# Performance work log

Hardware: AMD Instinct MI355X
Metric: run time of the kernel (lower is better)

## Reference

```python
import jax, jax.numpy as jnp
import numpy as np

B, E, D = 4096, 64, 1024

def setup_inputs() -> dict:
    key = jax.random.key(0)
    k1, k2 = jax.random.split(key)
    z = jax.random.normal(k1, (B, D), dtype=jnp.float32)
    expert_keys = jax.random.normal(k2, (E, D), dtype=jnp.float32)
    log_sigma = jnp.zeros((D,), dtype=jnp.float32)
    return {"z": z, "expert_keys": expert_keys, "log_sigma": log_sigma}

def reference(z, expert_keys, log_sigma):
    # diag(sigma_inv) @ diff followed by (. * diff).sum(-1) is exactly an
    # elementwise-scaled squared distance: sum_d exp(-log_sigma_d) * diff_d^2
    sigma_inv = jnp.exp(-log_sigma)                              # [D]
    diff = z[:, None, :] - expert_keys[None, :, :]               # [B, E, D]
    mahalanobis_dist = jnp.einsum('bed,d,bed->be', diff, sigma_inv, diff)  # [B, E]
    similarity = 1.0 / (1.0 + mahalanobis_dist)                  # [B, E]
    weights = jax.nn.softmax(similarity, axis=-1)                # [B, E]
    weighted_expert = weights @ expert_keys                      # [B, D]
    return (similarity, weighted_expert)
```

## Files before the change

### kernel.cpp

```cpp
#include <hip/hip_runtime.h>
#include <hip/hip_bf16.h>

#define B_N 4096
#define E_N 64
#define D_N 1024
#define ROWS 16

typedef __bf16 bf16x8 __attribute__((ext_vector_type(8)));
typedef __bf16 bf16x4 __attribute__((ext_vector_type(4)));
typedef float f32x4 __attribute__((ext_vector_type(4)));


__global__ __launch_bounds__(256) void prep_kernel(
    const float* __restrict__ keys, const float* __restrict__ lsig,
    float* __restrict__ sinv, float* __restrict__ ak,
    __bf16* __restrict__ sk, __bf16* __restrict__ kT)
{
  __shared__ float red[4];
  __shared__ __bf16 tl[64][72];
  const int bid = blockIdx.x;
  const int t = threadIdx.x;

  if (bid < 64) {
    const int e = bid;
    const float4 k4 = *(const float4*)(keys + e * D_N + 4 * t);
    const float4 l4 = *(const float4*)(lsig + 4 * t);
    float4 s4;
    s4.x = expf(-l4.x); s4.y = expf(-l4.y); s4.z = expf(-l4.z); s4.w = expf(-l4.w);
    if (e == 0) *(float4*)(sinv + 4 * t) = s4;
    const float4 sk4 = make_float4(s4.x * k4.x, s4.y * k4.y, s4.z * k4.z, s4.w * k4.w);
    bf16x4 skb;
    skb[0] = (__bf16)sk4.x; skb[1] = (__bf16)sk4.y; skb[2] = (__bf16)sk4.z; skb[3] = (__bf16)sk4.w;
    *(bf16x4*)(sk + e * D_N + 4 * t) = skb;
    float p = sk4.x * k4.x + sk4.y * k4.y + sk4.z * k4.z + sk4.w * k4.w;
    #pragma unroll
    for (int off = 32; off > 0; off >>= 1) p += __shfl_down(p, off);
    if ((t & 63) == 0) red[t >> 6] = p;
    __syncthreads();
    if (t == 0) ak[e] = red[0] + red[1] + red[2] + red[3];
  } else {
    const int d0 = (bid - 64) * 64;
    #pragma unroll
    for (int p = 0; p < 4; ++p) {
      const int e  = p * 16 + (t >> 4);
      const int dd = (t & 15) * 4;
      const float4 k4 = *(const float4*)(keys + (size_t)e * D_N + d0 + dd);
      tl[dd + 0][e] = (__bf16)k4.x; tl[dd + 1][e] = (__bf16)k4.y;
      tl[dd + 2][e] = (__bf16)k4.z; tl[dd + 3][e] = (__bf16)k4.w;
    }
    __syncthreads();
    #pragma unroll
    for (int p = 0; p < 2; ++p) {
      const int dd = p * 32 + (t >> 3);
      const int l8 = t & 7;
      const bf16x8 v = *(const bf16x8*)&tl[dd][l8 * 8];
      *(bf16x8*)(kT + (size_t)(d0 + dd) * E_N + l8 * 8) = v;
    }
  }
}

__global__ __launch_bounds__(256) void main_kernel(
    const float* __restrict__ z, const float* __restrict__ sinv,
    const float* __restrict__ ak, const __bf16* __restrict__ sk,
    const __bf16* __restrict__ kT,
    float* __restrict__ out_sim, float* __restrict__ out_we)
{
  constexpr int ZS = D_N + 8;
  __shared__ __bf16 zlds[ROWS * ZS];
  __shared__ float azs[ROWS];
  __shared__ float simb[ROWS][68];
  __shared__ __bf16 wlds[ROWS][72];

  const int t  = threadIdx.x;
  const int b0 = blockIdx.x * ROWS;
  const int wave = t >> 6;
  const int lane = t & 63;
  const int ln = lane & 15;
  const int q  = lane >> 4;

  const int sr = t >> 4;
  const int sc = t & 15;
  const float* zrow = z + (size_t)(b0 + sr) * D_N;
  float az = 0.f;
  #pragma unroll
  for (int l = 0; l < 8; ++l) {
    const int c = sc * 4 + l * 64;
    const float4 z4 = *(const float4*)(zrow + c);
    const float4 s4 = *(const float4*)(sinv + c);
    az += s4.x * z4.x * z4.x + s4.y * z4.y * z4.y + s4.z * z4.z * z4.z + s4.w * z4.w * z4.w;
    bf16x4 zb;
    zb[0] = (__bf16)z4.x; zb[1] = (__bf16)z4.y; zb[2] = (__bf16)z4.z; zb[3] = (__bf16)z4.w;
    *(bf16x4*)(&zlds[sr * ZS + c]) = zb;
  }
  const float akv = ak[wave * 16 + ln];
  __syncthreads();

  f32x4 acc = {0.f, 0.f, 0.f, 0.f};
  const __bf16* bp = sk + (size_t)(wave * 16 + ln) * D_N + q * 8;
  const __bf16* ap = &zlds[ln * ZS + q * 8];
  {
    float4 z4b[4], s4b[4];
    #pragma unroll
    for (int l = 0; l < 4; ++l) {
      const int c = 512 + sc * 4 + l * 64;
      z4b[l] = *(const float4*)(zrow + c);
      s4b[l] = *(const float4*)(sinv + c);
    }
    #pragma unroll
    for (int ks = 0; ks < 16; ++ks) {
      const bf16x8 bfr = *(const bf16x8*)(bp + ks * 32);
      const bf16x8 afr = *(const bf16x8*)(ap + ks * 32);
      acc = __builtin_amdgcn_mfma_f32_16x16x32_bf16(afr, bfr, acc, 0, 0, 0);
    }
    #pragma unroll
    for (int l = 0; l < 4; ++l) {
      const int c = 512 + sc * 4 + l * 64;
      const float4 z4 = z4b[l], s4 = s4b[l];
      az += s4.x * z4.x * z4.x + s4.y * z4.y * z4.y + s4.z * z4.z * z4.z + s4.w * z4.w * z4.w;
      bf16x4 zb;
      zb[0] = (__bf16)z4.x; zb[1] = (__bf16)z4.y; zb[2] = (__bf16)z4.z; zb[3] = (__bf16)z4.w;
      *(bf16x4*)(&zlds[sr * ZS + c]) = zb;
    }
    #pragma unroll
    for (int l = 0; l < 4; ++l) {
      const int c = 768 + sc * 4 + l * 64;
      const float4 z4 = *(const float4*)(zrow + c);
      const float4 s4 = *(const float4*)(sinv + c);
      az += s4.x * z4.x * z4.x + s4.y * z4.y * z4.y + s4.z * z4.z * z4.z + s4.w * z4.w * z4.w;
      bf16x4 zb;
      zb[0] = (__bf16)z4.x; zb[1] = (__bf16)z4.y; zb[2] = (__bf16)z4.z; zb[3] = (__bf16)z4.w;
      *(bf16x4*)(&zlds[sr * ZS + c]) = zb;
    }
  }
  az += __shfl_xor(az, 1); az += __shfl_xor(az, 2);
  az += __shfl_xor(az, 4); az += __shfl_xor(az, 8);
  if (sc == 0) azs[sr] = az;
  __syncthreads();

  #pragma unroll
  for (int ks = 16; ks < 32; ++ks) {
    const bf16x8 bfr = *(const bf16x8*)(bp + ks * 32);
    const bf16x8 afr = *(const bf16x8*)(ap + ks * 32);
    acc = __builtin_amdgcn_mfma_f32_16x16x32_bf16(afr, bfr, acc, 0, 0, 0);
  }
  #pragma unroll
  for (int i = 0; i < 4; ++i) {
    const int row = q * 4 + i;
    const float dist = azs[row] + akv - 2.0f * acc[i];
    simb[row][wave * 16 + ln] = 1.0f / (1.0f + dist);
  }
  const __bf16* kp0 = kT + (size_t)(wave * 256 + ln) * E_N + q * 8;
  const bf16x8 pa0 = *(const bf16x8*)(kp0);
  const bf16x8 pa1 = *(const bf16x8*)(kp0 + 32);
  __syncthreads();

  {
    const int row = wave * 4 + q;
    const f32x4 v4 = *(const f32x4*)&simb[row][ln * 4];
    float mx = fmaxf(fmaxf(v4[0], v4[1]), fmaxf(v4[2], v4[3]));
    mx = fmaxf(mx, __shfl_xor(mx, 1)); mx = fmaxf(mx, __shfl_xor(mx, 2));
    mx = fmaxf(mx, __shfl_xor(mx, 4)); mx = fmaxf(mx, __shfl_xor(mx, 8));
    float e0 = __expf(v4[0] - mx), e1 = __expf(v4[1] - mx);
    float e2 = __expf(v4[2] - mx), e3 = __expf(v4[3] - mx);
    float sum = e0 + e1 + e2 + e3;
    sum += __shfl_xor(sum, 1); sum += __shfl_xor(sum, 2);
    sum += __shfl_xor(sum, 4); sum += __shfl_xor(sum, 8);
    const float inv = 1.0f / sum;
    bf16x4 wv;
    wv[0] = (__bf16)(e0 * inv); wv[1] = (__bf16)(e1 * inv);
    wv[2] = (__bf16)(e2 * inv); wv[3] = (__bf16)(e3 * inv);
    *(bf16x4*)&wlds[row][ln * 4] = wv;
  }
  __syncthreads();

  {
    const float4 sv = *(const float4*)&simb[t >> 4][(t & 15) * 4];
    *(float4*)(out_sim + (size_t)(b0 + (t >> 4)) * E_N + (t & 15) * 4) = sv;
  }

  const bf16x8 wb0 = *(const bf16x8*)&wlds[ln][q * 8];
  const bf16x8 wb1 = *(const bf16x8*)&wlds[ln][32 + q * 8];
  float* orow = out_we + (size_t)(b0 + ln) * D_N + wave * 256 + q * 4;
  #pragma unroll
  for (int i = 0; i < 16; ++i) {
    const int d0 = wave * 256 + i * 16;
    bf16x8 a0f, a1f;
    if (i == 0) { a0f = pa0; a1f = pa1; }
    else {
      const __bf16* kp = kT + (size_t)(d0 + ln) * E_N + q * 8;
      a0f = *(const bf16x8*)(kp);
      a1f = *(const bf16x8*)(kp + 32);
    }
    f32x4 o = {0.f, 0.f, 0.f, 0.f};
    o = __builtin_amdgcn_mfma_f32_16x16x32_bf16(a0f, wb0, o, 0, 0, 0);
    o = __builtin_amdgcn_mfma_f32_16x16x32_bf16(a1f, wb1, o, 0, 0, 0);
    *(f32x4*)(orow + i * 16) = o;
  }
}

extern "C" void kernel_launch(void* const* d_in, const int* in_sizes, int n_in,
                              void* d_out, int out_size, void* d_ws, size_t ws_size,
                              hipStream_t stream)
{
  const float* z    = (const float*)d_in[0];
  const float* keys = (const float*)d_in[1];
  const float* ls   = (const float*)d_in[2];
  float* out_sim = (float*)d_out;
  float* out_we  = out_sim + (size_t)B_N * E_N;
  char* ws = (char*)d_ws;
  float*  sinv = (float*)(ws);
  float*  ak   = (float*)(ws + 4096);
  __bf16* sk   = (__bf16*)(ws + 4352);
  __bf16* kT   = (__bf16*)(ws + 135424);
  prep_kernel<<<80, 256, 0, stream>>>(keys, ls, sinv, ak, sk, kT);
  main_kernel<<<B_N / ROWS, 256, 0, stream>>>(z, sinv, ak, sk, kT, out_sim, out_we);
}
```

Measured before the change: 86.79 us.

## Simplify z staging to single pass and use nontemporal loads/stores for streams

Removes the split pipeline that overlapped loading the second half of z with the first half of the MFMA distance loop. All of z is now converted into LDS before a single barrier, followed by one 32-step MFMA loop. Streaming z reads and the similarity and weighted-output writes now use nontemporal hints to avoid polluting cache. This drops one barrier and some register buffering, but loses the load/compute overlap inside each block and relies on occupancy to hide latency.

New measurement: 84.32 us. -2.8%, faster.

```diff
diff --git a/kernel.cpp b/kernel.cpp
--- a/kernel.cpp
+++ b/kernel.cpp
@@ -83,62 +83,28 @@
   const float* zrow = z + (size_t)(b0 + sr) * D_N;
   float az = 0.f;
   #pragma unroll
-  for (int l = 0; l < 8; ++l) {
+  for (int l = 0; l < 16; ++l) {
     const int c = sc * 4 + l * 64;
-    const float4 z4 = *(const float4*)(zrow + c);
-    const float4 s4 = *(const float4*)(sinv + c);
-    az += s4.x * z4.x * z4.x + s4.y * z4.y * z4.y + s4.z * z4.z * z4.z + s4.w * z4.w * z4.w;
+    const f32x4 z4 = __builtin_nontemporal_load((const f32x4*)(zrow + c));
+    const f32x4 s4 = *(const f32x4*)(sinv + c);
+    az += s4[0] * z4[0] * z4[0] + s4[1] * z4[1] * z4[1]
+        + s4[2] * z4[2] * z4[2] + s4[3] * z4[3] * z4[3];
     bf16x4 zb;
-    zb[0] = (__bf16)z4.x; zb[1] = (__bf16)z4.y; zb[2] = (__bf16)z4.z; zb[3] = (__bf16)z4.w;
+    zb[0] = (__bf16)z4[0]; zb[1] = (__bf16)z4[1];
+    zb[2] = (__bf16)z4[2]; zb[3] = (__bf16)z4[3];
     *(bf16x4*)(&zlds[sr * ZS + c]) = zb;
   }
+  az += __shfl_xor(az, 1); az += __shfl_xor(az, 2);
+  az += __shfl_xor(az, 4); az += __shfl_xor(az, 8);
+  if (sc == 0) azs[sr] = az;
   const float akv = ak[wave * 16 + ln];
   __syncthreads();
 
   f32x4 acc = {0.f, 0.f, 0.f, 0.f};
   const __bf16* bp = sk + (size_t)(wave * 16 + ln) * D_N + q * 8;
   const __bf16* ap = &zlds[ln * ZS + q * 8];
-  {
-    float4 z4b[4], s4b[4];
-    #pragma unroll
-    for (int l = 0; l < 4; ++l) {
-      const int c = 512 + sc * 4 + l * 64;
-      z4b[l] = *(const float4*)(zrow + c);
-      s4b[l] = *(const float4*)(sinv + c);
-    }
-    #pragma unroll
-    for (int ks = 0; ks < 16; ++ks) {
-      const bf16x8 bfr = *(const bf16x8*)(bp + ks * 32);
-      const bf16x8 afr = *(const bf16x8*)(ap + ks * 32);
-      acc = __builtin_amdgcn_mfma_f32_16x16x32_bf16(afr, bfr, acc, 0, 0, 0);
-    }
-    #pragma unroll
-    for (int l = 0; l < 4; ++l) {
-      const int c = 512 + sc * 4 + l * 64;
-      const float4 z4 = z4b[l], s4 = s4b[l];
-      az += s4.x * z4.x * z4.x + s4.y * z4.y * z4.y + s4.z * z4.z * z4.z + s4.w * z4.w * z4.w;
-      bf16x4 zb;
-      zb[0] = (__bf16)z4.x; zb[1] = (__bf16)z4.y; zb[2] = (__bf16)z4.z; zb[3] = (__bf16)z4.w;
-      *(bf16x4*)(&zlds[sr * ZS + c]) = zb;
-    }
-    #pragma unroll
-    for (int l = 0; l < 4; ++l) {
-      const int c = 768 + sc * 4 + l * 64;
-      const float4 z4 = *(const float4*)(zrow + c);
-      const float4 s4 = *(const float4*)(sinv + c);
-      az += s4.x * z4.x * z4.x + s4.y * z4.y * z4.y + s4.z * z4.z * z4.z + s4.w * z4.w * z4.w;
-      bf16x4 zb;
-      zb[0] = (__bf16)z4.x; zb[1] = (__bf16)z4.y; zb[2] = (__bf16)z4.z; zb[3] = (__bf16)z4.w;
-      *(bf16x4*)(&zlds[sr * ZS + c]) = zb;
-    }
-  }
-  az += __shfl_xor(az, 1); az += __shfl_xor(az, 2);
-  az += __shfl_xor(az, 4); az += __shfl_xor(az, 8);
-  if (sc == 0) azs[sr] = az;
-  __syncthreads();
-
-  #pragma unroll
-  for (int ks = 16; ks < 32; ++ks) {
+  #pragma unroll 8
+  for (int ks = 0; ks < 32; ++ks) {
     const bf16x8 bfr = *(const bf16x8*)(bp + ks * 32);
     const bf16x8 afr = *(const bf16x8*)(ap + ks * 32);
     acc = __builtin_amdgcn_mfma_f32_16x16x32_bf16(afr, bfr, acc, 0, 0, 0);
@@ -174,8 +140,9 @@
   __syncthreads();
 
   {
-    const float4 sv = *(const float4*)&simb[t >> 4][(t & 15) * 4];
-    *(float4*)(out_sim + (size_t)(b0 + (t >> 4)) * E_N + (t & 15) * 4) = sv;
+    const f32x4 sv = *(const f32x4*)&simb[t >> 4][(t & 15) * 4];
+    __builtin_nontemporal_store(sv,
+        (f32x4*)(out_sim + (size_t)(b0 + (t >> 4)) * E_N + (t & 15) * 4));
   }
 
   const bf16x8 wb0 = *(const bf16x8*)&wlds[ln][q * 8];
@@ -194,7 +161,7 @@
     f32x4 o = {0.f, 0.f, 0.f, 0.f};
     o = __builtin_amdgcn_mfma_f32_16x16x32_bf16(a0f, wb0, o, 0, 0, 0);
     o = __builtin_amdgcn_mfma_f32_16x16x32_bf16(a1f, wb1, o, 0, 0, 0);
-    *(f32x4*)(orow + i * 16) = o;
+    __builtin_nontemporal_store(o, (f32x4*)(orow + i * 16));
   }
 }
 
```
